# Optimization experiments

Measured on AMD Instinct MI355X. Metric: run time of the kernel, lower is better.

Reference implementation:

```python
import jax, jax.numpy as jnp
import numpy as np

N_HEAD, D_MODEL, D_HEAD, D_INNER = 16, 1024, 64, 4096
QLEN, BSZ = 2048, 2
LN_EPS = 1e-5
NEG_MIN = np.float32(np.finfo(np.float32).min)


def layer_norm(x, g, b, eps=LN_EPS):
    mu = jnp.mean(x, axis=-1, keepdims=True)
    var = jnp.var(x, axis=-1, keepdims=True)
    return (x - mu) * jax.lax.rsqrt(var + eps) * g + b


def rel_shift_uni(x):
    # x: [q, k, b, n] -> Transformer-XL relative shift
    q, k, b, n = x.shape
    zero_pad = jnp.zeros((q, 1, b, n), dtype=x.dtype)
    x_padded = jnp.concatenate([zero_pad, x], axis=1)        # [q, k+1, b, n]
    x_padded = x_padded.reshape(k + 1, q, b, n)
    return x_padded[1:].reshape(q, k, b, n)


def setup_inputs() -> dict:
    key = jax.random.key(0)
    ks = jax.random.split(key, 16)
    s = 0.02
    inp = {
        "dec_inp": jax.random.normal(ks[0], (QLEN, BSZ, D_MODEL), jnp.float32),
        "r": jax.random.normal(ks[1], (QLEN, D_MODEL), jnp.float32),
        "r_w_bias": jax.random.normal(ks[2], (N_HEAD, D_HEAD), jnp.float32) * s,
        "r_r_bias": jax.random.normal(ks[3], (N_HEAD, D_HEAD), jnp.float32) * s,
        "qkv_w": jax.random.normal(ks[4], (3 * N_HEAD * D_HEAD, D_MODEL), jnp.float32) * s,
        "r_net_w": jax.random.normal(ks[5], (N_HEAD * D_HEAD, D_MODEL), jnp.float32) * s,
        "o_w": jax.random.normal(ks[6], (D_MODEL, N_HEAD * D_HEAD), jnp.float32) * s,
        "ln_attn_g": jnp.ones((D_MODEL,), jnp.float32),
        "ln_attn_b": jnp.zeros((D_MODEL,), jnp.float32),
        "w1": jax.random.normal(ks[7], (D_INNER, D_MODEL), jnp.float32) * s,
        "b1": jnp.zeros((D_INNER,), jnp.float32),
        "w2": jax.random.normal(ks[8], (D_MODEL, D_INNER), jnp.float32) * s,
        "b2": jnp.zeros((D_MODEL,), jnp.float32),
        "ln_ff_g": jnp.ones((D_MODEL,), jnp.float32),
        "ln_ff_b": jnp.zeros((D_MODEL,), jnp.float32),
        # causal mask: mask position j > i; shape [q, k, 1]
        "attn_mask": jnp.triu(jnp.ones((QLEN, QLEN), bool), k=1)[:, :, None],
    }
    return inp


def reference(dec_inp, r, r_w_bias, r_r_bias, qkv_w, r_net_w, o_w,
              ln_attn_g, ln_attn_b, w1, b1, w2, b2, ln_ff_g, ln_ff_b,
              attn_mask):
    qlen, bsz = dec_inp.shape[0], dec_inp.shape[1]
    scale = 1.0 / (D_HEAD ** 0.5)

    # QKV projection (post-LN: no pre-norm)
    w_heads = jnp.einsum('ibm,hm->ibh', dec_inp, qkv_w)  # [q, b, 3*n*d]
    w_head_q, w_head_k, w_head_v = jnp.split(w_heads, 3, axis=-1)
    w_head_q = w_head_q.reshape(qlen, bsz, N_HEAD, D_HEAD)
    w_head_k = w_head_k.reshape(qlen, bsz, N_HEAD, D_HEAD)
    w_head_v = w_head_v.reshape(qlen, bsz, N_HEAD, D_HEAD)

    # content attention score (AC)
    rw_head_q = w_head_q + r_w_bias                      # [q, b, n, d]
    attn_score = jnp.einsum('ibnd,jbnd->ijbn', rw_head_q, w_head_k)

    # position attention score (BD) with relative shift
    rr_head_q = w_head_q + r_r_bias
    r_head_k = jnp.einsum('jm,hm->jh', r, r_net_w).reshape(qlen, N_HEAD, D_HEAD)
    BD = jnp.einsum('ibnd,jnd->ijbn', rr_head_q, r_head_k)
    BD = rel_shift_uni(BD)

    attn_score = (attn_score + BD) * scale
    attn_score = jnp.where(attn_mask[:, :, :, None], NEG_MIN, attn_score)

    attn_prob = jax.nn.softmax(attn_score, axis=1)       # softmax over key dim
    attn_vec = jnp.einsum('ijbn,jbnd->ibnd', attn_prob, w_head_v)
    attn_vec = attn_vec.reshape(qlen, bsz, N_HEAD * D_HEAD)
    attn_out = jnp.einsum('ibh,mh->ibm', attn_vec, o_w)

    # post-LN residual
    output = layer_norm(dec_inp + attn_out, ln_attn_g, ln_attn_b)

    # Positionwise FFN (post-LN)
    hidden = jax.nn.relu(jnp.einsum('ibm,fm->ibf', output, w1) + b1)
    core_out = jnp.einsum('ibf,mf->ibm', hidden, w2) + b2
    output = layer_norm(output + core_out, ln_ff_g, ln_ff_b)
    return output
```

## Files before the change

kernel.cpp:

```cpp
#include <hip/hip_runtime.h>
#include <stdint.h>

#define QL 2048
#define NHEAD 16
#define DHEAD 64
#define DMODEL 1024
#define DINNER 4096

typedef __attribute__((ext_vector_type(8))) short bf16x8;
typedef __attribute__((ext_vector_type(4))) float f32x4;

template <bool V>
struct BoolC { static constexpr bool value = V; };

__device__ __forceinline__ ushort f2bf(float f) {
  uint32_t u = __float_as_uint(f);
  u = (u + 0x7fffu + ((u >> 16) & 1u)) >> 16;
  return (ushort)u;
}

__device__ __forceinline__ void gload_lds16(const void* g, void* l) {
  auto gp = reinterpret_cast<const uint32_t __attribute__((address_space(1)))*>(
      reinterpret_cast<uintptr_t>(g));
  auto lp = reinterpret_cast<uint32_t __attribute__((address_space(3)))*>(
      (uint32_t)reinterpret_cast<uintptr_t>(l));
  __builtin_amdgcn_global_load_lds(gp, lp, 16, 0, 0);
}

struct CvtArgs {
  const float* src[7];
  ushort* dst[7];
  int end[7];
};

__global__ __launch_bounds__(256) void cvt_all_k(CvtArgs a, int total4) {
  for (int i = blockIdx.x * 256 + threadIdx.x; i < total4; i += gridDim.x * 256) {
    int seg = 0;
#pragma unroll
    for (int s = 0; s < 6; s++)
      if (i >= a.end[s]) seg = s + 1;
    int base = seg ? a.end[seg - 1] : 0;
    int j = i - base;
    float4 v = ((const float4*)a.src[seg])[j];
    ushort4 u;
    u.x = f2bf(v.x); u.y = f2bf(v.y); u.z = f2bf(v.z); u.w = f2bf(v.w);
    ((ushort4*)a.dst[seg])[j] = u;
  }
}

#define EPI_QKV 0
#define EPI_RELU_BF16 3

#define QSCALE 0.18033688011112042f

template <int EPI>
__global__ __launch_bounds__(256) void gemm_nt(
    const ushort* __restrict__ A, const ushort* __restrict__ B, int M, int N, int K,
    float* __restrict__ Cf, ushort* __restrict__ Cb, const float* __restrict__ bias,
    ushort* __restrict__ qw, ushort* __restrict__ qr, ushort* __restrict__ kbuf,
    ushort* __restrict__ vt, const float* __restrict__ rwb, const float* __restrict__ rrb) {
  __shared__ ushort As[2][128 * 32];
  __shared__ ushort Bs[2][128 * 32];
  const int t = threadIdx.x;
  const int lane = t & 63, wv = t >> 6;
  const int wr = wv >> 1, wc = wv & 1;
  const int m0 = blockIdx.y * 128, n0 = blockIdx.x * 128;
  const int rif = lane & 15;
  const int kb = (lane >> 4) * 16;

  f32x4 acc[4][4] = {};
  const char* Ab = (const char*)A;
  const char* Bb = (const char*)B;
  const int arow = t >> 2;
  const int acol = (t & 3) * 16;

  auto stage = [&](int b, int k0) {
    size_t abase = ((size_t)(m0 + arow) * K + k0) * 2 + acol;
    gload_lds16(Ab + abase, (char*)As[b] + t * 16);
    gload_lds16(Ab + abase + (size_t)64 * K * 2, (char*)As[b] + t * 16 + 4096);
    size_t bbase = ((size_t)(n0 + arow) * K + k0) * 2 + acol;
    gload_lds16(Bb + bbase, (char*)Bs[b] + t * 16);
    gload_lds16(Bb + bbase + (size_t)64 * K * 2, (char*)Bs[b] + t * 16 + 4096);
  };

  stage(0, 0);
  asm volatile("s_waitcnt vmcnt(0)" ::: "memory");
  __builtin_amdgcn_s_barrier();
  __builtin_amdgcn_sched_barrier(0);

  int cur = 0;
#pragma unroll 1
  for (int k0 = 0; k0 < K; k0 += 32) {
    if (k0 + 32 < K) stage(cur ^ 1, k0 + 32);
    bf16x8 af[4], bfr[4];
#pragma unroll
    for (int m = 0; m < 4; m++)
      af[m] = *(const bf16x8*)((const char*)As[cur] + (wr * 64 + m * 16 + rif) * 64 + kb);
#pragma unroll
    for (int n = 0; n < 4; n++)
      bfr[n] = *(const bf16x8*)((const char*)Bs[cur] + (wc * 64 + n * 16 + rif) * 64 + kb);
    __builtin_amdgcn_s_setprio(1);
#pragma unroll
    for (int m = 0; m < 4; m++)
#pragma unroll
      for (int n = 0; n < 4; n++)
        acc[m][n] = __builtin_amdgcn_mfma_f32_16x16x32_bf16(af[m], bfr[n], acc[m][n], 0, 0, 0);
    __builtin_amdgcn_s_setprio(0);
    asm volatile("s_waitcnt vmcnt(0)" ::: "memory");
    __builtin_amdgcn_s_barrier();
    __builtin_amdgcn_sched_barrier(0);
    cur ^= 1;
  }

  const int rbase = (lane >> 4) * 4;
#pragma unroll
  for (int m = 0; m < 4; m++) {
#pragma unroll
    for (int n = 0; n < 4; n++) {
#pragma unroll
      for (int reg = 0; reg < 4; reg++) {
        int gr = m0 + wr * 64 + m * 16 + rbase + reg;
        int gc = n0 + wc * 64 + n * 16 + (lane & 15);
        float v = acc[m][n][reg];
        if (EPI == EPI_RELU_BF16) {
          Cb[(size_t)gr * N + gc] = f2bf(fmaxf(v + bias[gc], 0.f));
        } else {
          int which = gc >> 10, hh = gc & 1023;
          int hn = hh >> 6, hd = hh & 63;
          int qi = gr >> 1, qb = gr & 1;
          size_t off = ((size_t)(qb * NHEAD + hn) * QL + qi) * 64 + hd;
          if (which == 0) {
            qw[off] = f2bf((v + rwb[hh]) * QSCALE);
            qr[off] = f2bf((v + rrb[hh]) * QSCALE);
          } else if (which == 1) {
            kbuf[off] = f2bf(v);
          } else {
            vt[((size_t)(qb * NHEAD + hn) * 64 + hd) * QL + qi] = f2bf(v);
          }
        }
      }
    }
  }
}

template <int WITH_BIAS>
__global__ __launch_bounds__(256) void gemm_nt64sk(
    const ushort* __restrict__ A, const ushort* __restrict__ B, int M, int N, int Kfull,
    int Klen, float* __restrict__ Cf0, float* __restrict__ Cf1,
    const float* __restrict__ bias) {
  __shared__ ushort As[2][128 * 32];
  __shared__ ushort Bs[2][64 * 32];
  const int t = threadIdx.x;
  const int lane = t & 63, wv = t >> 6;
  const int wr = wv >> 1, wc = wv & 1;
  const int m0 = blockIdx.y * 128, n0 = blockIdx.x * 64;
  const int z = blockIdx.z;
  const int koff = z * Klen;
  float* Cf = z ? Cf1 : Cf0;
  const int rif = lane & 15;
  const int kb = (lane >> 4) * 16;

  f32x4 acc[4][2] = {};
  const char* Ab = (const char*)A;
  const char* Bb = (const char*)B;
  const int arow = t >> 2;
  const int acol = (t & 3) * 16;

  auto stage = [&](int b, int k0) {
    size_t abase = ((size_t)(m0 + arow) * Kfull + koff + k0) * 2 + acol;
    gload_lds16(Ab + abase, (char*)As[b] + t * 16);
    gload_lds16(Ab + abase + (size_t)64 * Kfull * 2, (char*)As[b] + t * 16 + 4096);
    size_t bbase = ((size_t)(n0 + arow) * Kfull + koff + k0) * 2 + acol;
    gload_lds16(Bb + bbase, (char*)Bs[b] + t * 16);
  };

  stage(0, 0);
  asm volatile("s_waitcnt vmcnt(0)" ::: "memory");
  __builtin_amdgcn_s_barrier();
  __builtin_amdgcn_sched_barrier(0);

  int cur = 0;
#pragma unroll 1
  for (int k0 = 0; k0 < Klen; k0 += 32) {
    if (k0 + 32 < Klen) stage(cur ^ 1, k0 + 32);
    bf16x8 af[4], bfr[2];
#pragma unroll
    for (int m = 0; m < 4; m++)
      af[m] = *(const bf16x8*)((const char*)As[cur] + (wr * 64 + m * 16 + rif) * 64 + kb);
#pragma unroll
    for (int n = 0; n < 2; n++)
      bfr[n] = *(const bf16x8*)((const char*)Bs[cur] + (wc * 32 + n * 16 + rif) * 64 + kb);
    __builtin_amdgcn_s_setprio(1);
#pragma unroll
    for (int m = 0; m < 4; m++)
#pragma unroll
      for (int n = 0; n < 2; n++)
        acc[m][n] = __builtin_amdgcn_mfma_f32_16x16x32_bf16(af[m], bfr[n], acc[m][n], 0, 0, 0);
    __builtin_amdgcn_s_setprio(0);
    asm volatile("s_waitcnt vmcnt(0)" ::: "memory");
    __builtin_amdgcn_s_barrier();
    __builtin_amdgcn_sched_barrier(0);
    cur ^= 1;
  }

  const int rbase = (lane >> 4) * 4;
#pragma unroll
  for (int m = 0; m < 4; m++) {
#pragma unroll
    for (int n = 0; n < 2; n++) {
#pragma unroll
      for (int reg = 0; reg < 4; reg++) {
        int gr = m0 + wr * 64 + m * 16 + rbase + reg;
        int gc = n0 + wc * 32 + n * 16 + (lane & 15);
        float v = acc[m][n][reg];
        if (WITH_BIAS && z == 0) v += bias[gc];
        Cf[(size_t)gr * N + gc] = v;
      }
    }
  }
}

__global__ __launch_bounds__(256) void gemm_rk64(
    const ushort* __restrict__ A, const ushort* __restrict__ B, int M, int N, int K,
    ushort* __restrict__ Cb) {
  __shared__ ushort As[2][64 * 32];
  __shared__ ushort Bs[2][64 * 32];
  const int t = threadIdx.x;
  const int lane = t & 63, wv = t >> 6;
  const int wr = wv >> 1, wc = wv & 1;
  const int m0 = blockIdx.y * 64, n0 = blockIdx.x * 64;
  const int rif = lane & 15;
  const int kb = (lane >> 4) * 16;

  f32x4 acc[2][2] = {};
  const char* Ab = (const char*)A;
  const char* Bb = (const char*)B;
  const int arow = t >> 2;
  const int acol = (t & 3) * 16;

  auto stage = [&](int b, int k0) {
    size_t abase = ((size_t)(m0 + arow) * K + k0) * 2 + acol;
    gload_lds16(Ab + abase, (char*)As[b] + t * 16);
    size_t bbase = ((size_t)(n0 + arow) * K + k0) * 2 + acol;
    gload_lds16(Bb + bbase, (char*)Bs[b] + t * 16);
  };

  stage(0, 0);
  asm volatile("s_waitcnt vmcnt(0)" ::: "memory");
  __builtin_amdgcn_s_barrier();
  __builtin_amdgcn_sched_barrier(0);

  int cur = 0;
#pragma unroll 1
  for (int k0 = 0; k0 < K; k0 += 32) {
    if (k0 + 32 < K) stage(cur ^ 1, k0 + 32);
    bf16x8 af[2], bfr[2];
#pragma unroll
    for (int m = 0; m < 2; m++)
      af[m] = *(const bf16x8*)((const char*)As[cur] + (wr * 32 + m * 16 + rif) * 64 + kb);
#pragma unroll
    for (int n = 0; n < 2; n++)
      bfr[n] = *(const bf16x8*)((const char*)Bs[cur] + (wc * 32 + n * 16 + rif) * 64 + kb);
    __builtin_amdgcn_s_setprio(1);
#pragma unroll
    for (int m = 0; m < 2; m++)
#pragma unroll
      for (int n = 0; n < 2; n++)
        acc[m][n] = __builtin_amdgcn_mfma_f32_16x16x32_bf16(af[m], bfr[n], acc[m][n], 0, 0, 0);
    __builtin_amdgcn_s_setprio(0);
    asm volatile("s_waitcnt vmcnt(0)" ::: "memory");
    __builtin_amdgcn_s_barrier();
    __builtin_amdgcn_sched_barrier(0);
    cur ^= 1;
  }

  const int rbase = (lane >> 4) * 4;
#pragma unroll
  for (int m = 0; m < 2; m++) {
#pragma unroll
    for (int n = 0; n < 2; n++) {
#pragma unroll
      for (int reg = 0; reg < 4; reg++) {
        int gr = m0 + wr * 32 + m * 16 + rbase + reg;
        int gc = n0 + wc * 32 + n * 16 + (lane & 15);
        int hn = gc >> 6, hd = gc & 63;
        Cb[((size_t)hn * QL + gr) * 64 + hd] = f2bf(acc[m][n][reg]);
      }
    }
  }
}

__global__ __launch_bounds__(256) void flash_attn(
    const ushort* __restrict__ Qw, const ushort* __restrict__ Qr,
    const ushort* __restrict__ Kb, const ushort* __restrict__ Vt,
    const ushort* __restrict__ Rk, ushort* __restrict__ out) {
  __shared__ ushort K_lds[2][64 * 64];
  __shared__ ushort V_lds[2][64 * 64];
  __shared__ ushort R_lds[2][128 * 64];
  __shared__ ushort P_lds[4][16 * 64];

  const int t = threadIdx.x;
  const int lane = t & 63, wv = t >> 6;
  const int bn = blockIdx.y;
  const int qb = bn >> 4, hn = bn & 15;
  const int c4 = lane & 15, g4 = lane >> 4;

  const char* Qwb = (const char*)(Qw + (size_t)bn * QL * 64);
  const char* Qrb = (const char*)(Qr + (size_t)bn * QL * 64);
  const char* Kbb = (const char*)(Kb + (size_t)bn * QL * 64);
  const char* Vtb = (const char*)(Vt + (size_t)bn * 64 * QL);
  const char* Rkb = (const char*)(Rk + (size_t)hn * QL * 64);

  int addrs[4];
#pragma unroll
  for (int reg = 0; reg < 4; reg++) {
    int rr = g4 * 4 + reg;
    addrs[reg] = ((lane & 48) | ((c4 + 15 - rr) & 15)) << 2;
  }

#pragma unroll 1
  for (int ph = 0; ph < 2; ph++) {
    const int itile = (ph == 0) ? (31 - (int)blockIdx.x) : (int)blockIdx.x;
    const int i0 = itile * 64;
    const int iw = i0 + wv * 16;
    const int niter = itile + 1;

    bf16x8 qwf[2], qrf[2];
#pragma unroll
    for (int kk = 0; kk < 2; kk++) {
      qwf[kk] = *(const bf16x8*)(Qwb + (size_t)(iw + c4) * 128 + kk * 64 + g4 * 16);
      qrf[kk] = *(const bf16x8*)(Qrb + (size_t)(iw + c4) * 128 + kk * 64 + g4 * 16);
    }

    f32x4 o_acc[4] = {};
    float m_run[4], l_run[4];
#pragma unroll
    for (int r = 0; r < 4; r++) { m_run[r] = -3.0e38f; l_run[r] = 0.f; }

    auto stage = [&](int b, int j0) {
      const int T0 = j0 - i0 + (QL - 64);
#pragma unroll
      for (int p = 0; p < 2; p++) {
        int o = t * 16 + p * 4096;
        int row = o >> 7, ch16 = ((((o & 127) >> 4) ^ (row & 7)) << 4);
        gload_lds16(Kbb + (size_t)(j0 + row) * 128 + ch16, (char*)K_lds[b] + o);
        gload_lds16(Vtb + (size_t)row * (QL * 2) + (size_t)j0 * 2 + ch16, (char*)V_lds[b] + o);
      }
#pragma unroll
      for (int p = 0; p < 4; p++) {
        int o = t * 16 + p * 4096;
        int r = o >> 7;
        int srow = T0 + r; srow = srow > QL - 1 ? QL - 1 : srow;
        int ch16 = ((((o & 127) >> 4) ^ (r & 7)) << 4);
        gload_lds16(Rkb + (size_t)srow * 128 + ch16, (char*)R_lds[b] + o);
      }
    };

    auto tile_body = [&](int j0, int cur, auto mc) {
      constexpr bool MASKED = decltype(mc)::value;
      f32x4 acc_s[4] = {};
      f32x4 acc_bd[5] = {};
      const int baseloc = 48 - wv * 16;
      __builtin_amdgcn_s_setprio(1);
#pragma unroll
      for (int kk = 0; kk < 2; kk++) {
        const int sw = (((kk * 4 + g4) ^ (c4 & 7)) << 4);
#pragma unroll
        for (int nf = 0; nf < 4; nf++) {
          bf16x8 bk = *(const bf16x8*)((const char*)K_lds[cur] + (nf * 16 + c4) * 128 + sw);
          acc_s[nf] = __builtin_amdgcn_mfma_f32_16x16x32_bf16(qwf[kk], bk, acc_s[nf], 0, 0, 0);
        }
#pragma unroll
        for (int tf = 0; tf < 5; tf++) {
          int oo = baseloc + tf * 16 + c4;
          bf16x8 br = *(const bf16x8*)((const char*)R_lds[cur] + oo * 128 + sw);
          acc_bd[tf] = __builtin_amdgcn_mfma_f32_16x16x32_bf16(qrf[kk], br, acc_bd[tf], 0, 0, 0);
        }
      }
      __builtin_amdgcn_s_setprio(0);

      uint32_t pk[4][4];
#pragma unroll
      for (int nf = 0; nf < 4; nf++)
#pragma unroll
        for (int reg = 0; reg < 4; reg++)
          asm("v_cvt_pk_bf16_f32 %0, %1, %2"
              : "=v"(pk[nf][reg])
              : "v"(acc_bd[nf][reg]), "v"(acc_bd[nf + 1][reg]));

      float sv[4][4];
      float rowmax[4] = {-3.0e38f, -3.0e38f, -3.0e38f, -3.0e38f};
#pragma unroll
      for (int nf = 0; nf < 4; nf++) {
#pragma unroll
        for (int reg = 0; reg < 4; reg++) {
          int rr = g4 * 4 + reg;
          uint32_t pulled = (uint32_t)__builtin_amdgcn_ds_bpermute(addrs[reg], (int)pk[nf][reg]);
          uint32_t bits = (c4 > rr) ? (pulled & 0xffff0000u) : (pulled << 16);
          float v = acc_s[nf][reg] + __uint_as_float(bits);
          if (MASKED) {
            int jg = j0 + nf * 16 + c4;
            int ig = iw + rr;
            v = (jg <= ig) ? v : -3.0e38f;
          }
          sv[nf][reg] = v;
          rowmax[reg] = fmaxf(rowmax[reg], v);
        }
      }
#pragma unroll
      for (int reg = 0; reg < 4; reg++) {
        float rm = rowmax[reg];
        rm = fmaxf(rm, __shfl_xor(rm, 1));
        rm = fmaxf(rm, __shfl_xor(rm, 2));
        rm = fmaxf(rm, __shfl_xor(rm, 4));
        rm = fmaxf(rm, __shfl_xor(rm, 8));
        float mnew = fmaxf(m_run[reg], rm);
        float alpha = __builtin_amdgcn_exp2f(m_run[reg] - mnew);
        float rsum = 0.f;
#pragma unroll
        for (int nf = 0; nf < 4; nf++) {
          float p = __builtin_amdgcn_exp2f(sv[nf][reg] - mnew);
          sv[nf][reg] = p;
          rsum += p;
        }
        rsum += __shfl_xor(rsum, 1);
        rsum += __shfl_xor(rsum, 2);
        rsum += __shfl_xor(rsum, 4);
        rsum += __shfl_xor(rsum, 8);
        l_run[reg] = l_run[reg] * alpha + rsum;
        m_run[reg] = mnew;
#pragma unroll
        for (int df = 0; df < 4; df++) o_acc[df][reg] *= alpha;
      }

      {
        char* pb = (char*)P_lds[wv];
#pragma unroll
        for (int nf = 0; nf < 4; nf++)
#pragma unroll
          for (int reg = 0; reg < 4; reg++) {
            int row = g4 * 4 + reg, col = nf * 16 + c4;
            int byt = row * 128 + ((((col >> 3) ^ (row & 7))) << 4) + (col & 7) * 2;
            *(ushort*)(pb + byt) = f2bf(sv[nf][reg]);
          }
      }
      __builtin_amdgcn_s_setprio(1);
#pragma unroll
      for (int kk = 0; kk < 2; kk++) {
        const char* pb = (const char*)P_lds[wv];
        bf16x8 pa = *(const bf16x8*)(pb + c4 * 128 + (((kk * 4 + g4) ^ (c4 & 7)) << 4));
        const int sw = (((kk * 4 + g4) ^ (c4 & 7)) << 4);
#pragma unroll
        for (int df = 0; df < 4; df++) {
          bf16x8 bv = *(const bf16x8*)((const char*)V_lds[cur] + (df * 16 + c4) * 128 + sw);
          o_acc[df] = __builtin_amdgcn_mfma_f32_16x16x32_bf16(pa, bv, o_acc[df], 0, 0, 0);
        }
      }
      __builtin_amdgcn_s_setprio(0);
    };

    stage(0, 0);
    asm volatile("s_waitcnt vmcnt(0)" ::: "memory");
    __builtin_amdgcn_s_barrier();
    __builtin_amdgcn_sched_barrier(0);

    int cur = 0;
#pragma unroll 1
    for (int it = 0; it < niter - 1; ++it) {
      stage(cur ^ 1, (it + 1) * 64);
      tile_body(it * 64, cur, BoolC<false>{});
      asm volatile("s_waitcnt vmcnt(0)" ::: "memory");
      __builtin_amdgcn_s_barrier();
      __builtin_amdgcn_sched_barrier(0);
      cur ^= 1;
    }
    tile_body(i0, cur, BoolC<true>{});
    __syncthreads();

#pragma unroll
    for (int reg = 0; reg < 4; reg++) {
      float inv = 1.0f / l_run[reg];
      int ig = iw + g4 * 4 + reg;
      size_t grow = (size_t)(ig * 2 + qb) * 1024 + hn * 64;
#pragma unroll
      for (int df = 0; df < 4; df++)
        out[grow + df * 16 + c4] = f2bf(o_acc[df][reg] * inv);
    }
  }
}

template <bool WB>
__global__ __launch_bounds__(256) void ln_res3(
    const float* __restrict__ xa, const float* __restrict__ xb0,
    const float* __restrict__ xb1, const float* __restrict__ g,
    const float* __restrict__ bt, float* __restrict__ of, ushort* __restrict__ ob) {
  __shared__ float red[8];
  const int row = blockIdx.x;
  const int t = threadIdx.x;
  const int lane = t & 63, wv = t >> 6;
  const float4 a = *(const float4*)(xa + (size_t)row * 1024 + t * 4);
  const float4 c0 = *(const float4*)(xb0 + (size_t)row * 1024 + t * 4);
  const float4 c1 = *(const float4*)(xb1 + (size_t)row * 1024 + t * 4);
  float x[4] = {a.x + c0.x + c1.x, a.y + c0.y + c1.y, a.z + c0.z + c1.z, a.w + c0.w + c1.w};
  float s = x[0] + x[1] + x[2] + x[3];
  for (int m = 1; m < 64; m <<= 1) s += __shfl_xor(s, m);
  if (lane == 0) red[wv] = s;
  __syncthreads();
  float mu = (red[0] + red[1] + red[2] + red[3]) * (1.f / 1024.f);
  float d[4];
  float ss = 0.f;
#pragma unroll
  for (int i = 0; i < 4; i++) { d[i] = x[i] - mu; ss += d[i] * d[i]; }
  for (int m = 1; m < 64; m <<= 1) ss += __shfl_xor(ss, m);
  if (lane == 0) red[4 + wv] = ss;
  __syncthreads();
  float var = (red[4] + red[5] + red[6] + red[7]) * (1.f / 1024.f);
  float rs = rsqrtf(var + 1e-5f);
  float4 gv = *(const float4*)(g + t * 4);
  float4 bv = *(const float4*)(bt + t * 4);
  float y[4] = {d[0] * rs * gv.x + bv.x, d[1] * rs * gv.y + bv.y,
                d[2] * rs * gv.z + bv.z, d[3] * rs * gv.w + bv.w};
  float4 yo = make_float4(y[0], y[1], y[2], y[3]);
  *(float4*)(of + (size_t)row * 1024 + t * 4) = yo;
  if (WB) {
    ushort4 u;
    u.x = f2bf(y[0]); u.y = f2bf(y[1]); u.z = f2bf(y[2]); u.w = f2bf(y[3]);
    *(ushort4*)(ob + (size_t)row * 1024 + t * 4) = u;
  }
}

extern "C" void kernel_launch(void* const* d_in, const int* in_sizes, int n_in,
                              void* d_out, int out_size, void* d_ws, size_t ws_size,
                              hipStream_t stream) {
  const float* dec_inp = (const float*)d_in[0];
  const float* r_in = (const float*)d_in[1];
  const float* rwb = (const float*)d_in[2];
  const float* rrb = (const float*)d_in[3];
  const float* qkv_w = (const float*)d_in[4];
  const float* rnet_w = (const float*)d_in[5];
  const float* o_w = (const float*)d_in[6];
  const float* ln_attn_g = (const float*)d_in[7];
  const float* ln_attn_b = (const float*)d_in[8];
  const float* w1 = (const float*)d_in[9];
  const float* b1 = (const float*)d_in[10];
  const float* w2 = (const float*)d_in[11];
  const float* b2 = (const float*)d_in[12];
  const float* ln_ff_g = (const float*)d_in[13];
  const float* ln_ff_b = (const float*)d_in[14];
  float* out = (float*)d_out;

  char* ws = (char*)d_ws;
  size_t off = 0;
  auto alloc = [&](size_t bytes) {
    char* p = ws + off;
    off += (bytes + 255) & ~(size_t)255;
    return p;
  };
  const int ROWS = QL * 2;
  ushort* qkvw_b = (ushort*)alloc((size_t)3072 * 1024 * 2);
  ushort* rnetw_b = (ushort*)alloc((size_t)1024 * 1024 * 2);
  ushort* ow_b = (ushort*)alloc((size_t)1024 * 1024 * 2);
  ushort* w1_b = (ushort*)alloc((size_t)4096 * 1024 * 2);
  ushort* w2_b = (ushort*)alloc((size_t)1024 * 4096 * 2);
  ushort* x_b = (ushort*)alloc((size_t)ROWS * 1024 * 2);
  ushort* r_b = (ushort*)alloc((size_t)QL * 1024 * 2);
  ushort* Qw = (ushort*)alloc((size_t)32 * QL * 64 * 2);
  ushort* Qr = (ushort*)alloc((size_t)32 * QL * 64 * 2);
  ushort* Kb = (ushort*)alloc((size_t)32 * QL * 64 * 2);
  ushort* Vt = (ushort*)alloc((size_t)32 * 64 * QL * 2);
  ushort* rk = (ushort*)alloc((size_t)16 * QL * 64 * 2);
  ushort* avec = (ushort*)alloc((size_t)ROWS * 1024 * 2);
  float* p0 = (float*)alloc((size_t)ROWS * 1024 * 4);
  float* p1 = (float*)alloc((size_t)ROWS * 1024 * 4);
  float* x1f = (float*)alloc((size_t)ROWS * 1024 * 4);
  ushort* x1b = (ushort*)alloc((size_t)ROWS * 1024 * 2);
  ushort* hidden = (ushort*)alloc((size_t)ROWS * 4096 * 2);
  float* q0 = (float*)alloc((size_t)ROWS * 1024 * 4);
  float* q1 = (float*)alloc((size_t)ROWS * 1024 * 4);

  CvtArgs ca;
  int n4[7] = {3072 * 1024 / 4, 1024 * 1024 / 4, 1024 * 1024 / 4, 4096 * 1024 / 4,
               1024 * 4096 / 4, ROWS * 1024 / 4, QL * 1024 / 4};
  const float* srcs[7] = {qkv_w, rnet_w, o_w, w1, w2, dec_inp, r_in};
  ushort* dsts[7] = {qkvw_b, rnetw_b, ow_b, w1_b, w2_b, x_b, r_b};
  int cum = 0;
  for (int i = 0; i < 7; i++) {
    ca.src[i] = srcs[i];
    ca.dst[i] = dsts[i];
    cum += n4[i];
    ca.end[i] = cum;
  }
  cvt_all_k<<<2048, 256, 0, stream>>>(ca, cum);

  gemm_nt<EPI_QKV><<<dim3(3072 / 128, ROWS / 128), 256, 0, stream>>>(
      x_b, qkvw_b, ROWS, 3072, 1024, nullptr, nullptr, nullptr, Qw, Qr, Kb, Vt, rwb, rrb);
  gemm_rk64<<<dim3(1024 / 64, QL / 64), 256, 0, stream>>>(r_b, rnetw_b, QL, 1024, 1024, rk);
  flash_attn<<<dim3(16, 32), 256, 0, stream>>>(Qw, Qr, Kb, Vt, rk, avec);
  gemm_nt64sk<0><<<dim3(1024 / 64, ROWS / 128, 2), 256, 0, stream>>>(
      avec, ow_b, ROWS, 1024, 1024, 512, p0, p1, nullptr);
  ln_res3<true><<<ROWS, 256, 0, stream>>>(dec_inp, p0, p1, ln_attn_g, ln_attn_b, x1f, x1b);
  gemm_nt<EPI_RELU_BF16><<<dim3(4096 / 128, ROWS / 128), 256, 0, stream>>>(
      x1b, w1_b, ROWS, 4096, 1024, nullptr, hidden, b1, nullptr, nullptr, nullptr, nullptr,
      nullptr, nullptr);
  gemm_nt64sk<1><<<dim3(1024 / 64, ROWS / 128, 2), 256, 0, stream>>>(
      hidden, w2_b, ROWS, 1024, 4096, 2048, q0, q1, b2);
  ln_res3<false><<<ROWS, 256, 0, stream>>>(x1f, q0, q1, ln_ff_g, ln_ff_b, out, nullptr);
}
```

Before: 345.5 us.

## Fuse QKV, r-net GEMMs and late weight casts into one launch; bf16 split-K partials

The QKV projection GEMM, the r_net projection GEMM and the cast of o_w/w1/w2 to bf16 now run as one kernel. Block-index ranges pick the role, so the three kinds of work share the GPU and launches are removed. The first conversion kernel now only casts the tensors needed by the QKV/r-net GEMMs. Split-K partial outputs of the o-proj and FFN2 GEMMs are stored as bf16 instead of fp32, halving that traffic. This costs precision in the residual sum before LayerNorm, and the fused kernel's shared-memory size fixes occupancy for every role.

```diff
diff --git a/kernel.cpp b/kernel.cpp
--- a/kernel.cpp
+++ b/kernel.cpp
@@ -17,6 +17,9 @@
   uint32_t u = __float_as_uint(f);
   u = (u + 0x7fffu + ((u >> 16) & 1u)) >> 16;
   return (ushort)u;
+}
+__device__ __forceinline__ float bf2f(ushort u) {
+  return __uint_as_float(((uint32_t)u) << 16);
 }
 
 __device__ __forceinline__ void gload_lds16(const void* g, void* l) {
@@ -27,17 +30,19 @@
   __builtin_amdgcn_global_load_lds(gp, lp, 16, 0, 0);
 }
 
+#define QSCALE 0.18033688011112042f
+
 struct CvtArgs {
-  const float* src[7];
-  ushort* dst[7];
-  int end[7];
+  const float* src[4];
+  ushort* dst[4];
+  int end[4];
 };
 
 __global__ __launch_bounds__(256) void cvt_all_k(CvtArgs a, int total4) {
   for (int i = blockIdx.x * 256 + threadIdx.x; i < total4; i += gridDim.x * 256) {
     int seg = 0;
 #pragma unroll
-    for (int s = 0; s < 6; s++)
+    for (int s = 0; s < 3; s++)
       if (i >= a.end[s]) seg = s + 1;
     int base = seg ? a.end[seg - 1] : 0;
     int j = i - base;
@@ -48,83 +53,89 @@
   }
 }
 
-#define EPI_QKV 0
-#define EPI_RELU_BF16 3
-
-#define QSCALE 0.18033688011112042f
-
-template <int EPI>
-__global__ __launch_bounds__(256) void gemm_nt(
-    const ushort* __restrict__ A, const ushort* __restrict__ B, int M, int N, int K,
-    float* __restrict__ Cf, ushort* __restrict__ Cb, const float* __restrict__ bias,
+struct Cvt3 {
+  const float* src[3];
+  ushort* dst[3];
+  int end[3];
+};
+
+__global__ __launch_bounds__(256) void fat_qkv_rk_cvt(
+    const ushort* __restrict__ xb, const ushort* __restrict__ qkvw,
+    const ushort* __restrict__ rb, const ushort* __restrict__ rnetw,
     ushort* __restrict__ qw, ushort* __restrict__ qr, ushort* __restrict__ kbuf,
-    ushort* __restrict__ vt, const float* __restrict__ rwb, const float* __restrict__ rrb) {
-  __shared__ ushort As[2][128 * 32];
-  __shared__ ushort Bs[2][128 * 32];
+    ushort* __restrict__ vt, ushort* __restrict__ rkout,
+    const float* __restrict__ rwb, const float* __restrict__ rrb,
+    Cvt3 cv, int cvt_total4) {
+  __shared__ char smem[32768];
+  const int bid = blockIdx.x;
   const int t = threadIdx.x;
   const int lane = t & 63, wv = t >> 6;
   const int wr = wv >> 1, wc = wv & 1;
-  const int m0 = blockIdx.y * 128, n0 = blockIdx.x * 128;
   const int rif = lane & 15;
   const int kb = (lane >> 4) * 16;
-
-  f32x4 acc[4][4] = {};
-  const char* Ab = (const char*)A;
-  const char* Bb = (const char*)B;
   const int arow = t >> 2;
   const int acol = (t & 3) * 16;
-
-  auto stage = [&](int b, int k0) {
-    size_t abase = ((size_t)(m0 + arow) * K + k0) * 2 + acol;
-    gload_lds16(Ab + abase, (char*)As[b] + t * 16);
-    gload_lds16(Ab + abase + (size_t)64 * K * 2, (char*)As[b] + t * 16 + 4096);
-    size_t bbase = ((size_t)(n0 + arow) * K + k0) * 2 + acol;
-    gload_lds16(Bb + bbase, (char*)Bs[b] + t * 16);
-    gload_lds16(Bb + bbase + (size_t)64 * K * 2, (char*)Bs[b] + t * 16 + 4096);
-  };
-
-  stage(0, 0);
-  asm volatile("s_waitcnt vmcnt(0)" ::: "memory");
-  __builtin_amdgcn_s_barrier();
-  __builtin_amdgcn_sched_barrier(0);
-
-  int cur = 0;
-#pragma unroll 1
-  for (int k0 = 0; k0 < K; k0 += 32) {
-    if (k0 + 32 < K) stage(cur ^ 1, k0 + 32);
-    bf16x8 af[4], bfr[4];
-#pragma unroll
-    for (int m = 0; m < 4; m++)
-      af[m] = *(const bf16x8*)((const char*)As[cur] + (wr * 64 + m * 16 + rif) * 64 + kb);
-#pragma unroll
-    for (int n = 0; n < 4; n++)
-      bfr[n] = *(const bf16x8*)((const char*)Bs[cur] + (wc * 64 + n * 16 + rif) * 64 + kb);
-    __builtin_amdgcn_s_setprio(1);
-#pragma unroll
-    for (int m = 0; m < 4; m++)
-#pragma unroll
-      for (int n = 0; n < 4; n++)
-        acc[m][n] = __builtin_amdgcn_mfma_f32_16x16x32_bf16(af[m], bfr[n], acc[m][n], 0, 0, 0);
-    __builtin_amdgcn_s_setprio(0);
+  const int rbase = (lane >> 4) * 4;
+
+  if (bid < 768) {
+    const int bx = bid % 24, by = bid / 24;
+    const int m0 = by * 128, n0 = bx * 128;
+    const int K = 1024;
+    const char* Ab = (const char*)xb;
+    const char* Bb = (const char*)qkvw;
+
+    f32x4 acc[4][4] = {};
+    auto stage = [&](int b, int k0) {
+      char* As = smem + b * 8192;
+      char* Bs = smem + 16384 + b * 8192;
+      size_t abase = ((size_t)(m0 + arow) * K + k0) * 2 + acol;
+      gload_lds16(Ab + abase, As + t * 16);
+      gload_lds16(Ab + abase + (size_t)64 * K * 2, As + t * 16 + 4096);
+      size_t bbase = ((size_t)(n0 + arow) * K + k0) * 2 + acol;
+      gload_lds16(Bb + bbase, Bs + t * 16);
+      gload_lds16(Bb + bbase + (size_t)64 * K * 2, Bs + t * 16 + 4096);
+    };
+
+    stage(0, 0);
     asm volatile("s_waitcnt vmcnt(0)" ::: "memory");
     __builtin_amdgcn_s_barrier();
     __builtin_amdgcn_sched_barrier(0);
-    cur ^= 1;
-  }
-
-  const int rbase = (lane >> 4) * 4;
-#pragma unroll
-  for (int m = 0; m < 4; m++) {
-#pragma unroll
-    for (int n = 0; n < 4; n++) {
-#pragma unroll
-      for (int reg = 0; reg < 4; reg++) {
-        int gr = m0 + wr * 64 + m * 16 + rbase + reg;
-        int gc = n0 + wc * 64 + n * 16 + (lane & 15);
-        float v = acc[m][n][reg];
-        if (EPI == EPI_RELU_BF16) {
-          Cb[(size_t)gr * N + gc] = f2bf(fmaxf(v + bias[gc], 0.f));
-        } else {
+
+    int cur = 0;
+#pragma unroll 1
+    for (int k0 = 0; k0 < K; k0 += 32) {
+      if (k0 + 32 < K) stage(cur ^ 1, k0 + 32);
+      const char* As = smem + cur * 8192;
+      const char* Bs = smem + 16384 + cur * 8192;
+      bf16x8 af[4], bfr[4];
+#pragma unroll
+      for (int m = 0; m < 4; m++)
+        af[m] = *(const bf16x8*)(As + (wr * 64 + m * 16 + rif) * 64 + kb);
+#pragma unroll
+      for (int n = 0; n < 4; n++)
+        bfr[n] = *(const bf16x8*)(Bs + (wc * 64 + n * 16 + rif) * 64 + kb);
+      __builtin_amdgcn_s_setprio(1);
+#pragma unroll
+      for (int m = 0; m < 4; m++)
+#pragma unroll
+        for (int n = 0; n < 4; n++)
+          acc[m][n] = __builtin_amdgcn_mfma_f32_16x16x32_bf16(af[m], bfr[n], acc[m][n], 0, 0, 0);
+      __builtin_amdgcn_s_setprio(0);
+      asm volatile("s_waitcnt vmcnt(0)" ::: "memory");
+      __builtin_amdgcn_s_barrier();
+      __builtin_amdgcn_sched_barrier(0);
+      cur ^= 1;
+    }
+
+#pragma unroll
+    for (int m = 0; m < 4; m++) {
+#pragma unroll
+      for (int n = 0; n < 4; n++) {
+#pragma unroll
+        for (int reg = 0; reg < 4; reg++) {
+          int gr = m0 + wr * 64 + m * 16 + rbase + reg;
+          int gc = n0 + wc * 64 + n * 16 + (lane & 15);
+          float v = acc[m][n][reg];
           int which = gc >> 10, hh = gc & 1023;
           int hn = hh >> 6, hd = hh & 63;
           int qi = gr >> 1, qb = gr & 1;
@@ -140,13 +151,159 @@
         }
       }
     }
+  } else if (bid < 1280) {
+    const int b = bid - 768;
+    const int bx = b % 16, by = b / 16;
+    const int m0 = by * 64, n0 = bx * 64;
+    const int K = 1024;
+    const char* Ab = (const char*)rb;
+    const char* Bb = (const char*)rnetw;
+
+    f32x4 acc[2][2] = {};
+    auto stage = [&](int bb, int k0) {
+      char* As = smem + bb * 4096;
+      char* Bs = smem + 8192 + bb * 4096;
+      size_t abase = ((size_t)(m0 + arow) * K + k0) * 2 + acol;
+      gload_lds16(Ab + abase, As + t * 16);
+      size_t bbase = ((size_t)(n0 + arow) * K + k0) * 2 + acol;
+      gload_lds16(Bb + bbase, Bs + t * 16);
+    };
+
+    stage(0, 0);
+    asm volatile("s_waitcnt vmcnt(0)" ::: "memory");
+    __builtin_amdgcn_s_barrier();
+    __builtin_amdgcn_sched_barrier(0);
+
+    int cur = 0;
+#pragma unroll 1
+    for (int k0 = 0; k0 < K; k0 += 32) {
+      if (k0 + 32 < K) stage(cur ^ 1, k0 + 32);
+      const char* As = smem + cur * 4096;
+      const char* Bs = smem + 8192 + cur * 4096;
+      bf16x8 af[2], bfr[2];
+#pragma unroll
+      for (int m = 0; m < 2; m++)
+        af[m] = *(const bf16x8*)(As + (wr * 32 + m * 16 + rif) * 64 + kb);
+#pragma unroll
+      for (int n = 0; n < 2; n++)
+        bfr[n] = *(const bf16x8*)(Bs + (wc * 32 + n * 16 + rif) * 64 + kb);
+      __builtin_amdgcn_s_setprio(1);
+#pragma unroll
+      for (int m = 0; m < 2; m++)
+#pragma unroll
+        for (int n = 0; n < 2; n++)
+          acc[m][n] = __builtin_amdgcn_mfma_f32_16x16x32_bf16(af[m], bfr[n], acc[m][n], 0, 0, 0);
+      __builtin_amdgcn_s_setprio(0);
+      asm volatile("s_waitcnt vmcnt(0)" ::: "memory");
+      __builtin_amdgcn_s_barrier();
+      __builtin_amdgcn_sched_barrier(0);
+      cur ^= 1;
+    }
+
+#pragma unroll
+    for (int m = 0; m < 2; m++) {
+#pragma unroll
+      for (int n = 0; n < 2; n++) {
+#pragma unroll
+        for (int reg = 0; reg < 4; reg++) {
+          int gr = m0 + wr * 32 + m * 16 + rbase + reg;
+          int gc = n0 + wc * 32 + n * 16 + (lane & 15);
+          int hn = gc >> 6, hd = gc & 63;
+          rkout[((size_t)hn * QL + gr) * 64 + hd] = f2bf(acc[m][n][reg]);
+        }
+      }
+    }
+  } else {
+    for (int i = (bid - 1280) * 256 + t; i < cvt_total4; i += 512 * 256) {
+      int seg = 0;
+#pragma unroll
+      for (int s = 0; s < 2; s++)
+        if (i >= cv.end[s]) seg = s + 1;
+      int base = seg ? cv.end[seg - 1] : 0;
+      int j = i - base;
+      float4 v = ((const float4*)cv.src[seg])[j];
+      ushort4 u;
+      u.x = f2bf(v.x); u.y = f2bf(v.y); u.z = f2bf(v.z); u.w = f2bf(v.w);
+      ((ushort4*)cv.dst[seg])[j] = u;
+    }
+  }
+}
+
+__global__ __launch_bounds__(256) void gemm_ffn1(
+    const ushort* __restrict__ A, const ushort* __restrict__ B, int M, int N, int K,
+    ushort* __restrict__ Cb, const float* __restrict__ bias) {
+  __shared__ ushort As[2][128 * 32];
+  __shared__ ushort Bs[2][128 * 32];
+  const int t = threadIdx.x;
+  const int lane = t & 63, wv = t >> 6;
+  const int wr = wv >> 1, wc = wv & 1;
+  const int m0 = blockIdx.y * 128, n0 = blockIdx.x * 128;
+  const int rif = lane & 15;
+  const int kb = (lane >> 4) * 16;
+
+  f32x4 acc[4][4] = {};
+  const char* Ab = (const char*)A;
+  const char* Bb = (const char*)B;
+  const int arow = t >> 2;
+  const int acol = (t & 3) * 16;
+
+  auto stage = [&](int b, int k0) {
+    size_t abase = ((size_t)(m0 + arow) * K + k0) * 2 + acol;
+    gload_lds16(Ab + abase, (char*)As[b] + t * 16);
+    gload_lds16(Ab + abase + (size_t)64 * K * 2, (char*)As[b] + t * 16 + 4096);
+    size_t bbase = ((size_t)(n0 + arow) * K + k0) * 2 + acol;
+    gload_lds16(Bb + bbase, (char*)Bs[b] + t * 16);
+    gload_lds16(Bb + bbase + (size_t)64 * K * 2, (char*)Bs[b] + t * 16 + 4096);
+  };
+
+  stage(0, 0);
+  asm volatile("s_waitcnt vmcnt(0)" ::: "memory");
+  __builtin_amdgcn_s_barrier();
+  __builtin_amdgcn_sched_barrier(0);
+
+  int cur = 0;
+#pragma unroll 1
+  for (int k0 = 0; k0 < K; k0 += 32) {
+    if (k0 + 32 < K) stage(cur ^ 1, k0 + 32);
+    bf16x8 af[4], bfr[4];
+#pragma unroll
+    for (int m = 0; m < 4; m++)
+      af[m] = *(const bf16x8*)((const char*)As[cur] + (wr * 64 + m * 16 + rif) * 64 + kb);
+#pragma unroll
+    for (int n = 0; n < 4; n++)
+      bfr[n] = *(const bf16x8*)((const char*)Bs[cur] + (wc * 64 + n * 16 + rif) * 64 + kb);
+    __builtin_amdgcn_s_setprio(1);
+#pragma unroll
+    for (int m = 0; m < 4; m++)
+#pragma unroll
+      for (int n = 0; n < 4; n++)
+        acc[m][n] = __builtin_amdgcn_mfma_f32_16x16x32_bf16(af[m], bfr[n], acc[m][n], 0, 0, 0);
+    __builtin_amdgcn_s_setprio(0);
+    asm volatile("s_waitcnt vmcnt(0)" ::: "memory");
+    __builtin_amdgcn_s_barrier();
+    __builtin_amdgcn_sched_barrier(0);
+    cur ^= 1;
+  }
+
+  const int rbase = (lane >> 4) * 4;
+#pragma unroll
+  for (int m = 0; m < 4; m++) {
+#pragma unroll
+    for (int n = 0; n < 4; n++) {
+#pragma unroll
+      for (int reg = 0; reg < 4; reg++) {
+        int gr = m0 + wr * 64 + m * 16 + rbase + reg;
+        int gc = n0 + wc * 64 + n * 16 + (lane & 15);
+        Cb[(size_t)gr * N + gc] = f2bf(fmaxf(acc[m][n][reg] + bias[gc], 0.f));
+      }
+    }
   }
 }
 
 template <int WITH_BIAS>
 __global__ __launch_bounds__(256) void gemm_nt64sk(
     const ushort* __restrict__ A, const ushort* __restrict__ B, int M, int N, int Kfull,
-    int Klen, float* __restrict__ Cf0, float* __restrict__ Cf1,
+    int Klen, ushort* __restrict__ Cb0, ushort* __restrict__ Cb1,
     const float* __restrict__ bias) {
   __shared__ ushort As[2][128 * 32];
   __shared__ ushort Bs[2][64 * 32];
@@ -156,7 +313,7 @@
   const int m0 = blockIdx.y * 128, n0 = blockIdx.x * 64;
   const int z = blockIdx.z;
   const int koff = z * Klen;
-  float* Cf = z ? Cf1 : Cf0;
+  ushort* Cb = z ? Cb1 : Cb0;
   const int rif = lane & 15;
   const int kb = (lane >> 4) * 16;
 
@@ -214,77 +371,7 @@
         int gc = n0 + wc * 32 + n * 16 + (lane & 15);
         float v = acc[m][n][reg];
         if (WITH_BIAS && z == 0) v += bias[gc];
-        Cf[(size_t)gr * N + gc] = v;
-      }
-    }
-  }
-}
-
-__global__ __launch_bounds__(256) void gemm_rk64(
-    const ushort* __restrict__ A, const ushort* __restrict__ B, int M, int N, int K,
-    ushort* __restrict__ Cb) {
-  __shared__ ushort As[2][64 * 32];
-  __shared__ ushort Bs[2][64 * 32];
-  const int t = threadIdx.x;
-  const int lane = t & 63, wv = t >> 6;
-  const int wr = wv >> 1, wc = wv & 1;
-  const int m0 = blockIdx.y * 64, n0 = blockIdx.x * 64;
-  const int rif = lane & 15;
-  const int kb = (lane >> 4) * 16;
-
-  f32x4 acc[2][2] = {};
-  const char* Ab = (const char*)A;
-  const char* Bb = (const char*)B;
-  const int arow = t >> 2;
-  const int acol = (t & 3) * 16;
-
-  auto stage = [&](int b, int k0) {
-    size_t abase = ((size_t)(m0 + arow) * K + k0) * 2 + acol;
-    gload_lds16(Ab + abase, (char*)As[b] + t * 16);
-    size_t bbase = ((size_t)(n0 + arow) * K + k0) * 2 + acol;
-    gload_lds16(Bb + bbase, (char*)Bs[b] + t * 16);
-  };
-
-  stage(0, 0);
-  asm volatile("s_waitcnt vmcnt(0)" ::: "memory");
-  __builtin_amdgcn_s_barrier();
-  __builtin_amdgcn_sched_barrier(0);
-
-  int cur = 0;
-#pragma unroll 1
-  for (int k0 = 0; k0 < K; k0 += 32) {
-    if (k0 + 32 < K) stage(cur ^ 1, k0 + 32);
-    bf16x8 af[2], bfr[2];
-#pragma unroll
-    for (int m = 0; m < 2; m++)
-      af[m] = *(const bf16x8*)((const char*)As[cur] + (wr * 32 + m * 16 + rif) * 64 + kb);
-#pragma unroll
-    for (int n = 0; n < 2; n++)
-      bfr[n] = *(const bf16x8*)((const char*)Bs[cur] + (wc * 32 + n * 16 + rif) * 64 + kb);
-    __builtin_amdgcn_s_setprio(1);
-#pragma unroll
-    for (int m = 0; m < 2; m++)
-#pragma unroll
-      for (int n = 0; n < 2; n++)
-        acc[m][n] = __builtin_amdgcn_mfma_f32_16x16x32_bf16(af[m], bfr[n], acc[m][n], 0, 0, 0);
-    __builtin_amdgcn_s_setprio(0);
-    asm volatile("s_waitcnt vmcnt(0)" ::: "memory");
-    __builtin_amdgcn_s_barrier();
-    __builtin_amdgcn_sched_barrier(0);
-    cur ^= 1;
-  }
-
-  const int rbase = (lane >> 4) * 4;
-#pragma unroll
-  for (int m = 0; m < 2; m++) {
-#pragma unroll
-    for (int n = 0; n < 2; n++) {
-#pragma unroll
-      for (int reg = 0; reg < 4; reg++) {
-        int gr = m0 + wr * 32 + m * 16 + rbase + reg;
-        int gc = n0 + wc * 32 + n * 16 + (lane & 15);
-        int hn = gc >> 6, hd = gc & 63;
-        Cb[((size_t)hn * QL + gr) * 64 + hd] = f2bf(acc[m][n][reg]);
+        Cb[(size_t)gr * N + gc] = f2bf(v);
       }
     }
   }
@@ -491,17 +578,18 @@
 
 template <bool WB>
 __global__ __launch_bounds__(256) void ln_res3(
-    const float* __restrict__ xa, const float* __restrict__ xb0,
-    const float* __restrict__ xb1, const float* __restrict__ g,
+    const float* __restrict__ xa, const ushort* __restrict__ xb0,
+    const ushort* __restrict__ xb1, const float* __restrict__ g,
     const float* __restrict__ bt, float* __restrict__ of, ushort* __restrict__ ob) {
   __shared__ float red[8];
   const int row = blockIdx.x;
   const int t = threadIdx.x;
   const int lane = t & 63, wv = t >> 6;
   const float4 a = *(const float4*)(xa + (size_t)row * 1024 + t * 4);
-  const float4 c0 = *(const float4*)(xb0 + (size_t)row * 1024 + t * 4);
-  const float4 c1 = *(const float4*)(xb1 + (size_t)row * 1024 + t * 4);
-  float x[4] = {a.x + c0.x + c1.x, a.y + c0.y + c1.y, a.z + c0.z + c1.z, a.w + c0.w + c1.w};
+  const ushort4 c0 = *(const ushort4*)(xb0 + (size_t)row * 1024 + t * 4);
+  const ushort4 c1 = *(const ushort4*)(xb1 + (size_t)row * 1024 + t * 4);
+  float x[4] = {a.x + bf2f(c0.x) + bf2f(c1.x), a.y + bf2f(c0.y) + bf2f(c1.y),
+                a.z + bf2f(c0.z) + bf2f(c1.z), a.w + bf2f(c0.w) + bf2f(c1.w)};
   float s = x[0] + x[1] + x[2] + x[3];
   for (int m = 1; m < 64; m <<= 1) s += __shfl_xor(s, m);
   if (lane == 0) red[wv] = s;
@@ -570,38 +658,53 @@
   ushort* Vt = (ushort*)alloc((size_t)32 * 64 * QL * 2);
   ushort* rk = (ushort*)alloc((size_t)16 * QL * 64 * 2);
   ushort* avec = (ushort*)alloc((size_t)ROWS * 1024 * 2);
-  float* p0 = (float*)alloc((size_t)ROWS * 1024 * 4);
-  float* p1 = (float*)alloc((size_t)ROWS * 1024 * 4);
+  ushort* p0 = (ushort*)alloc((size_t)ROWS * 1024 * 2);
+  ushort* p1 = (ushort*)alloc((size_t)ROWS * 1024 * 2);
   float* x1f = (float*)alloc((size_t)ROWS * 1024 * 4);
   ushort* x1b = (ushort*)alloc((size_t)ROWS * 1024 * 2);
   ushort* hidden = (ushort*)alloc((size_t)ROWS * 4096 * 2);
-  float* q0 = (float*)alloc((size_t)ROWS * 1024 * 4);
-  float* q1 = (float*)alloc((size_t)ROWS * 1024 * 4);
+  ushort* q0 = (ushort*)alloc((size_t)ROWS * 1024 * 2);
+  ushort* q1 = (ushort*)alloc((size_t)ROWS * 1024 * 2);
 
   CvtArgs ca;
-  int n4[7] = {3072 * 1024 / 4, 1024 * 1024 / 4, 1024 * 1024 / 4, 4096 * 1024 / 4,
-               1024 * 4096 / 4, ROWS * 1024 / 4, QL * 1024 / 4};
-  const float* srcs[7] = {qkv_w, rnet_w, o_w, w1, w2, dec_inp, r_in};
-  ushort* dsts[7] = {qkvw_b, rnetw_b, ow_b, w1_b, w2_b, x_b, r_b};
-  int cum = 0;
-  for (int i = 0; i < 7; i++) {
-    ca.src[i] = srcs[i];
-    ca.dst[i] = dsts[i];
-    cum += n4[i];
-    ca.end[i] = cum;
-  }
-  cvt_all_k<<<2048, 256, 0, stream>>>(ca, cum);
-
-  gemm_nt<EPI_QKV><<<dim3(3072 / 128, ROWS / 128), 256, 0, stream>>>(
-      x_b, qkvw_b, ROWS, 3072, 1024, nullptr, nullptr, nullptr, Qw, Qr, Kb, Vt, rwb, rrb);
-  gemm_rk64<<<dim3(1024 / 64, QL / 64), 256, 0, stream>>>(r_b, rnetw_b, QL, 1024, 1024, rk);
+  {
+    int n4[4] = {3072 * 1024 / 4, 1024 * 1024 / 4, ROWS * 1024 / 4, QL * 1024 / 4};
+    const float* srcs[4] = {qkv_w, rnet_w, dec_inp, r_in};
+    ushort* dsts[4] = {qkvw_b, rnetw_b, x_b, r_b};
+    int cum = 0;
+    for (int i = 0; i < 4; i++) {
+      ca.src[i] = srcs[i];
+      ca.dst[i] = dsts[i];
+      cum += n4[i];
+      ca.end[i] = cum;
+    }
+    cvt_all_k<<<2048, 256, 0, stream>>>(ca, cum);
+  }
+
+  Cvt3 cv;
+  int cvt_total4;
+  {
+    int n4[3] = {1024 * 1024 / 4, 4096 * 1024 / 4, 1024 * 4096 / 4};
+    const float* srcs[3] = {o_w, w1, w2};
+    ushort* dsts[3] = {ow_b, w1_b, w2_b};
+    int cum = 0;
+    for (int i = 0; i < 3; i++) {
+      cv.src[i] = srcs[i];
+      cv.dst[i] = dsts[i];
+      cum += n4[i];
+      cv.end[i] = cum;
+    }
+    cvt_total4 = cum;
+  }
+  fat_qkv_rk_cvt<<<1792, 256, 0, stream>>>(x_b, qkvw_b, r_b, rnetw_b, Qw, Qr, Kb, Vt, rk,
+                                           rwb, rrb, cv, cvt_total4);
+
   flash_attn<<<dim3(16, 32), 256, 0, stream>>>(Qw, Qr, Kb, Vt, rk, avec);
   gemm_nt64sk<0><<<dim3(1024 / 64, ROWS / 128, 2), 256, 0, stream>>>(
       avec, ow_b, ROWS, 1024, 1024, 512, p0, p1, nullptr);
   ln_res3<true><<<ROWS, 256, 0, stream>>>(dec_inp, p0, p1, ln_attn_g, ln_attn_b, x1f, x1b);
-  gemm_nt<EPI_RELU_BF16><<<dim3(4096 / 128, ROWS / 128), 256, 0, stream>>>(
-      x1b, w1_b, ROWS, 4096, 1024, nullptr, hidden, b1, nullptr, nullptr, nullptr, nullptr,
-      nullptr, nullptr);
+  gemm_ffn1<<<dim3(4096 / 128, ROWS / 128), 256, 0, stream>>>(
+      x1b, w1_b, ROWS, 4096, 1024, hidden, b1);
   gemm_nt64sk<1><<<dim3(1024 / 64, ROWS / 128, 2), 256, 0, stream>>>(
       hidden, w2_b, ROWS, 1024, 4096, 2048, q0, q1, b2);
   ln_res3<false><<<ROWS, 256, 0, stream>>>(x1f, q0, q1, ln_ff_g, ln_ff_b, out, nullptr);
```

New measurement: 336.1 us, median of 2. 1.03x faster.
